# Kernel tuning notes

Measured on AMD Instinct MI355X. Metric: run time of the kernel, lower is better.

## Reference

```python
import jax, jax.numpy as jnp
import numpy as np

B, T, D_IN = 8, 1024, 320
L, H, DK, DV, DM, DI = 6, 8, 64, 64, 512, 2048


def _pe_table():
    pos = np.arange(T, dtype=np.float32)[:, None]
    div = np.exp(np.arange(0, DM, 2, dtype=np.float32) * (-np.log(10000.0) / DM))
    pe = np.zeros((T, DM), np.float32)
    pe[:, 0::2] = np.sin(pos * div)
    pe[:, 1::2] = np.cos(pos * div)
    return jnp.asarray(pe)


def setup_inputs() -> dict:
    key = jax.random.key(0)
    ks = jax.random.split(key, 16)
    rn = lambda k, shape, std: (jax.random.normal(k, shape, jnp.float32) * std)
    inp = {}
    inp["padded_input"] = jax.random.normal(ks[0], (B, T, D_IN), jnp.float32)
    inp["input_lengths"] = jax.random.randint(ks[1], (B,), T // 2, T + 1)
    # input projection + input layernorm (weights stored as [in, out])
    inp["w_in"] = rn(ks[2], (D_IN, DM), 0.02)
    inp["b_in"] = jnp.zeros((DM,), jnp.float32)
    inp["ln_in_g"] = jnp.ones((DM,), jnp.float32)
    inp["ln_in_b"] = jnp.zeros((DM,), jnp.float32)
    inp["pe"] = _pe_table()
    # stacked per-layer params, leading dim L
    inp["wq"] = rn(ks[3], (L, DM, H * DK), np.sqrt(2.0 / (DM + DK)))
    inp["bq"] = jnp.zeros((L, H * DK), jnp.float32)
    inp["wk"] = rn(ks[4], (L, DM, H * DK), np.sqrt(2.0 / (DM + DK)))
    inp["bk"] = jnp.zeros((L, H * DK), jnp.float32)
    inp["wv"] = rn(ks[5], (L, DM, H * DV), np.sqrt(2.0 / (DM + DV)))
    inp["bv"] = jnp.zeros((L, H * DV), jnp.float32)
    inp["wfc"] = rn(ks[6], (L, H * DV, DM), np.sqrt(2.0 / (H * DV + DM)))
    inp["bfc"] = jnp.zeros((L, DM), jnp.float32)
    inp["ln1_g"] = jnp.ones((L, DM), jnp.float32)
    inp["ln1_b"] = jnp.zeros((L, DM), jnp.float32)
    inp["w1"] = rn(ks[7], (L, DM, DI), np.sqrt(2.0 / (DM + DI)))
    inp["b1"] = jnp.zeros((L, DI), jnp.float32)
    inp["w2"] = rn(ks[8], (L, DI, DM), np.sqrt(2.0 / (DM + DI)))
    inp["b2"] = jnp.zeros((L, DM), jnp.float32)
    inp["ln2_g"] = jnp.ones((L, DM), jnp.float32)
    inp["ln2_b"] = jnp.zeros((L, DM), jnp.float32)
    return inp


def _layer_norm(x, g, b):
    mu = jnp.mean(x, axis=-1, keepdims=True)
    var = jnp.var(x, axis=-1, keepdims=True)
    return (x - mu) * jax.lax.rsqrt(var + 1e-5) * g + b


def _encoder(padded_input, input_lengths, w_in, b_in, ln_in_g, ln_in_b, pe,
             wq, bq, wk, bk, wv, bv, wfc, bfc, ln1_g, ln1_b,
             w1, b1, w2, b2, ln2_g, ln2_b):
    pos = jnp.arange(T)
    key_pad = pos[None, :] >= input_lengths[:, None]          # [B,T] True at pad
    non_pad = (~key_pad).astype(padded_input.dtype)[:, :, None]  # [B,T,1]
    scale = 1.0 / jnp.sqrt(jnp.float32(DK))

    x = _layer_norm(padded_input @ w_in + b_in, ln_in_g, ln_in_b) + pe[None]

    def body(x, p):
        Wq, Bq, Wk, Bk, Wv, Bv, Wfc, Bfc, G1, Bn1, W1, Bf1, W2, Bf2, G2, Bn2 = p
        res = x
        q = (x @ Wq + Bq).reshape(B, T, H, DK)
        k = (x @ Wk + Bk).reshape(B, T, H, DK)
        v = (x @ Wv + Bv).reshape(B, T, H, DV)
        attn = jnp.einsum('bqhd,bkhd->bhqk', q, k) * scale
        attn = jnp.where(key_pad[:, None, None, :], -jnp.inf, attn)
        attn = jax.nn.softmax(attn, axis=-1)
        o = jnp.einsum('bhqk,bkhd->bqhd', attn, v).reshape(B, T, H * DV)
        x = _layer_norm(o @ Wfc + Bfc + res, G1, Bn1) * non_pad
        res = x
        h = jax.nn.relu(x @ W1 + Bf1)
        x = _layer_norm(h @ W2 + Bf2 + res, G2, Bn2) * non_pad
        return x, None

    x, _ = jax.lax.scan(body, x, (wq, bq, wk, bk, wv, bv, wfc, bfc,
                                  ln1_g, ln1_b, w1, b1, w2, b2, ln2_g, ln2_b))
    return x


def reference(padded_input, input_lengths, w_in, b_in, ln_in_g, ln_in_b, pe,
              wq, bq, wk, bk, wv, bv, wfc, bfc, ln1_g, ln1_b,
              w1, b1, w2, b2, ln2_g, ln2_b):
    # dropout is identity in eval mode
    return _encoder(padded_input, input_lengths, w_in, b_in, ln_in_g, ln_in_b, pe,
                    wq, bq, wk, bk, wv, bv, wfc, bfc, ln1_g, ln1_b,
                    w1, b1, w2, b2, ln2_g, ln2_b)
```

## Files before the change

### kernel.cpp

```cpp
#include <hip/hip_runtime.h>
#include <hip/hip_bf16.h>


typedef unsigned short bh16;
typedef __bf16 bf16x8 __attribute__((ext_vector_type(8)));
typedef float f32x4 __attribute__((ext_vector_type(4)));
typedef unsigned int u32x4 __attribute__((ext_vector_type(4)));
typedef unsigned int u32x2 __attribute__((ext_vector_type(2)));

#define DEVI static __device__ __forceinline__

DEVI bh16 f2bf(float f) {
  union { float f; unsigned u; } x; x.f = f;
  unsigned r = x.u + 0x7fffu + ((x.u >> 16) & 1u);
  return (bh16)(r >> 16);
}
DEVI float bf2f(bh16 u) {
  union { unsigned u; float f; } x; x.u = ((unsigned)u) << 16; return x.f;
}
DEVI bf16x8 ld16(const bh16* p) {
  return __builtin_bit_cast(bf16x8, *(const u32x4*)p);
}
DEVI bf16x8 ld16b(const char* p) {
  return __builtin_bit_cast(bf16x8, *(const u32x4*)p);
}
DEVI f32x4 mfma16(bf16x8 a, bf16x8 b, f32x4 c) {
  return __builtin_amdgcn_mfma_f32_16x16x32_bf16(a, b, c, 0, 0, 0);
}
DEVI void async16(const void* g, void* l) {
  __builtin_amdgcn_global_load_lds(
      (const __attribute__((address_space(1))) void*)g,
      (__attribute__((address_space(3))) void*)l, 16, 0, 0);
}

__global__ __launch_bounds__(256) void tcvt(
    const float* __restrict__ in, bh16* __restrict__ out,
    int K, int N, long long inLS, long long outLS, int rowOff) {
  int l = blockIdx.z;
  in += (size_t)l * inLS;
  out += (size_t)l * outLS + (size_t)rowOff * K;
  __shared__ float t[32][33];
  int n0 = blockIdx.x * 32, k0 = blockIdx.y * 32;
  int tx = threadIdx.x & 31, ty = threadIdx.x >> 5;
#pragma unroll
  for (int i = 0; i < 4; i++)
    t[ty + 8 * i][tx] = in[(size_t)(k0 + ty + 8 * i) * N + n0 + tx];
  __syncthreads();
#pragma unroll
  for (int i = 0; i < 4; i++)
    out[(size_t)(n0 + ty + 8 * i) * K + k0 + tx] = f2bf(t[tx][ty + 8 * i]);
}

__global__ __launch_bounds__(256) void bcat(
    const float* __restrict__ bq, const float* __restrict__ bk,
    const float* __restrict__ bv, float* __restrict__ out) {
  int l = blockIdx.x;
  for (int j = threadIdx.x; j < 1536; j += 256) {
    float v = (j < 512) ? bq[l * 512 + j]
            : (j < 1024) ? bk[l * 512 + j - 512] : bv[l * 512 + j - 1024];
    out[l * 1536 + j] = v;
  }
}

__global__ __launch_bounds__(256) void cvt_in(
    const float* __restrict__ in, bh16* __restrict__ out, int n4) {
  int i = blockIdx.x * 256 + threadIdx.x;
  if (i < n4) {
    float4 v = ((const float4*)in)[i];
    u32x2 pk;
    pk[0] = (unsigned)f2bf(v.x) | ((unsigned)f2bf(v.y) << 16);
    pk[1] = (unsigned)f2bf(v.z) | ((unsigned)f2bf(v.w) << 16);
    *(u32x2*)(out + (size_t)i * 4) = pk;
  }
}

template <int RELU, int OUTF32, int QKV>
__global__ __launch_bounds__(256) void gemm_bt(
    const bh16* __restrict__ A, const bh16* __restrict__ Bt,
    const float* __restrict__ bias, void* __restrict__ Cout,
    bh16* __restrict__ vtOut, int M, int N, int K) {
  constexpr int BM = 128, BN = 64, BK = 64;
  __shared__ __align__(16) bh16 As[3][BM * BK];
  __shared__ __align__(16) bh16 Bs[3][BN * BK];
  const int tid = threadIdx.x;
  const int wave = tid >> 6, lane = tid & 63;
  const int lq = lane & 15, grp = lane >> 4;
  const int p = blockIdx.x;
  const int xcd = p & 7, idx = p >> 3;
  const int m0 = (((xcd << 3) | (idx & 7))) * BM;
  const int n0 = (idx >> 3) * BN;
  constexpr int FM = BM / 32, FN = BN / 32;
  const int wr = wave >> 1, wc = wave & 1;
  f32x4 acc[FM][FN] = {};

  const int nk = K / BK;
  auto stage = [&](int buf, int kt) {
#pragma unroll
    for (int i = 0; i < BM / 32; ++i) {
      int off = i * 4096 + wave * 1024 + lane * 16;
      int row = off >> 7, col = off & 127;
      int sw = (row & 7) << 4;
      const char* g =
          (const char*)A + ((size_t)(m0 + row) * K + kt * BK) * 2 + (col ^ sw);
      async16(g, (char*)As[buf] + off);
    }
#pragma unroll
    for (int i = 0; i < BN / 32; ++i) {
      int off = i * 4096 + wave * 1024 + lane * 16;
      int row = off >> 7, col = off & 127;
      int sw = (row & 7) << 4;
      const char* g =
          (const char*)Bt + ((size_t)(n0 + row) * K + kt * BK) * 2 + (col ^ sw);
      async16(g, (char*)Bs[buf] + off);
    }
  };

  stage(0, 0);
  stage(1, 1);
  int cur = 0, nxt = 2;
  for (int kt = 0; kt < nk; ++kt) {
    asm volatile("s_waitcnt vmcnt(6)" ::: "memory");
    __builtin_amdgcn_s_barrier();
    __builtin_amdgcn_sched_barrier(0);
    if (kt + 2 < nk) stage(nxt, kt + 2);
#pragma unroll
    for (int kk = 0; kk < 2; ++kk) {
      bf16x8 af[FM], bfr[FN];
#pragma unroll
      for (int i = 0; i < FM; ++i) {
        int row = wr * (BM / 2) + i * 16 + lq;
        int sw = (row & 7) << 4;
        af[i] = ld16b((char*)As[cur] + row * 128 + ((kk * 64 + grp * 16) ^ sw));
      }
#pragma unroll
      for (int j = 0; j < FN; ++j) {
        int row = wc * (BN / 2) + j * 16 + lq;
        int sw = (row & 7) << 4;
        bfr[j] = ld16b((char*)Bs[cur] + row * 128 + ((kk * 64 + grp * 16) ^ sw));
      }
      __builtin_amdgcn_s_setprio(1);
#pragma unroll
      for (int i = 0; i < FM; ++i)
#pragma unroll
        for (int j = 0; j < FN; ++j)
          acc[i][j] = mfma16(af[i], bfr[j], acc[i][j]);
      __builtin_amdgcn_s_setprio(0);
    }
    cur = (cur == 2) ? 0 : cur + 1;
    nxt = (nxt == 2) ? 0 : nxt + 1;
  }
  if (QKV && n0 >= 1024) {
#pragma unroll
    for (int i = 0; i < FM; ++i) {
#pragma unroll
      for (int j = 0; j < FN; ++j) {
        int col = n0 + wc * (BN / 2) + j * 16 + lq;
        float bv = bias[col];
        int vc = col - 1024;
        int t0 = m0 + wr * (BM / 2) + i * 16 + grp * 4;
        int bb = t0 >> 10, tl = t0 & 1023;
        u32x2 pk;
        pk[0] = (unsigned)f2bf(acc[i][j][0] + bv) |
                ((unsigned)f2bf(acc[i][j][1] + bv) << 16);
        pk[1] = (unsigned)f2bf(acc[i][j][2] + bv) |
                ((unsigned)f2bf(acc[i][j][3] + bv) << 16);
        *(u32x2*)&vtOut[((size_t)(bb * 512 + vc)) * 1024 + tl] = pk;
      }
    }
    return;
  }
#pragma unroll
  for (int i = 0; i < FM; ++i) {
#pragma unroll
    for (int j = 0; j < FN; ++j) {
      int col = n0 + wc * (BN / 2) + j * 16 + lq;
      float bv = bias[col];
#pragma unroll
      for (int r = 0; r < 4; ++r) {
        int row = m0 + wr * (BM / 2) + i * 16 + grp * 4 + r;
        float v = acc[i][j][r] + bv;
        if (RELU) v = fmaxf(v, 0.f);
        if (OUTF32) ((float*)Cout)[(size_t)row * N + col] = v;
        else ((bh16*)Cout)[(size_t)row * N + col] = f2bf(v);
      }
    }
  }
}

__global__ __launch_bounds__(256) void ln_pe_k(
    const float* __restrict__ in, const float* __restrict__ g,
    const float* __restrict__ bta, const float* __restrict__ pe,
    bh16* __restrict__ xb) {
  int wave = threadIdx.x >> 6, lane = threadIdx.x & 63;
  int row = blockIdx.x * 4 + wave;
  int t = row & 1023;
  const float* xr = in + (size_t)row * 512 + lane * 8;
  float4 a0 = ((const float4*)xr)[0], a1 = ((const float4*)xr)[1];
  float v[8] = {a0.x, a0.y, a0.z, a0.w, a1.x, a1.y, a1.z, a1.w};
  float s = 0.f, ss = 0.f;
#pragma unroll
  for (int j = 0; j < 8; j++) { s += v[j]; ss += v[j] * v[j]; }
#pragma unroll
  for (int m = 1; m < 64; m <<= 1) { s += __shfl_xor(s, m); ss += __shfl_xor(ss, m); }
  float mu = s * (1.f / 512.f);
  float rstd = rsqrtf(ss * (1.f / 512.f) - mu * mu + 1e-5f);
  int c0 = lane * 8;
  float o[8];
  u32x4 pk;
#pragma unroll
  for (int j = 0; j < 8; j++) {
    int c = c0 + j;
    o[j] = (v[j] - mu) * rstd * g[c] + bta[c] + pe[(size_t)t * 512 + c];
  }
#pragma unroll
  for (int j = 0; j < 4; j++)
    pk[j] = (unsigned)f2bf(o[2 * j]) | ((unsigned)f2bf(o[2 * j + 1]) << 16);
  *(u32x4*)(xb + (size_t)row * 512 + c0) = pk;
}

__global__ __launch_bounds__(256) void ln_res_k(
    const bh16* __restrict__ gout, const bh16* res,
    const float* __restrict__ g, const float* __restrict__ bta,
    const int* __restrict__ lens, bh16* xb, float* fout) {
  int wave = threadIdx.x >> 6, lane = threadIdx.x & 63;
  int row = blockIdx.x * 4 + wave;
  int b = row >> 10, t = row & 1023;
  float nonpad = (t < lens[b]) ? 1.f : 0.f;
  int c0 = lane * 8;
  u32x4 graw = *(const u32x4*)(gout + (size_t)row * 512 + c0);
  u32x4 rraw = *(const u32x4*)(res + (size_t)row * 512 + c0);
  float v[8];
#pragma unroll
  for (int j = 0; j < 4; j++) {
    v[2 * j] = bf2f((bh16)(graw[j] & 0xffffu)) + bf2f((bh16)(rraw[j] & 0xffffu));
    v[2 * j + 1] = bf2f((bh16)(graw[j] >> 16)) + bf2f((bh16)(rraw[j] >> 16));
  }
  float s = 0.f, ss = 0.f;
#pragma unroll
  for (int j = 0; j < 8; j++) { s += v[j]; ss += v[j] * v[j]; }
#pragma unroll
  for (int m = 1; m < 64; m <<= 1) { s += __shfl_xor(s, m); ss += __shfl_xor(ss, m); }
  float mu = s * (1.f / 512.f);
  float rstd = rsqrtf(ss * (1.f / 512.f) - mu * mu + 1e-5f);
  float o[8];
  u32x4 pk;
#pragma unroll
  for (int j = 0; j < 8; j++) {
    int c = c0 + j;
    o[j] = ((v[j] - mu) * rstd * g[c] + bta[c]) * nonpad;
  }
#pragma unroll
  for (int j = 0; j < 4; j++)
    pk[j] = (unsigned)f2bf(o[2 * j]) | ((unsigned)f2bf(o[2 * j + 1]) << 16);
  *(u32x4*)(xb + (size_t)row * 512 + c0) = pk;
  if (fout) {
    float4* xo = (float4*)(fout + (size_t)row * 512 + c0);
    xo[0] = make_float4(o[0], o[1], o[2], o[3]);
    xo[1] = make_float4(o[4], o[5], o[6], o[7]);
  }
}

__global__ __launch_bounds__(512) void attn_k(
    const bh16* __restrict__ qkv, const bh16* __restrict__ vt,
    const int* __restrict__ lens, bh16* __restrict__ o) {
  constexpr int LDP = 72;
  __shared__ __align__(16) char Ks[2][8192];
  __shared__ __align__(16) char Vs[2][8192];
  __shared__ __align__(16) bh16 P[8][16 * LDP];
  int p = blockIdx.x;
  int xcd = p & 7, s = p >> 3;
  int bh = ((s & 7) << 3) | xcd;
  int qt = s >> 3;
  int b = bh >> 3, h = bh & 7;
  int len = lens[b];
  if (qt * 128 >= len) return;
  int tid = threadIdx.x;
  int wave = tid >> 6, lane = tid & 63;
  int lq = lane & 15, grp = lane >> 4;

  size_t qrow = (size_t)(b * 1024 + qt * 128 + wave * 16 + lq);
  const bh16* Qp = qkv + qrow * 1536 + h * 64;
  bf16x8 qf0 = ld16(Qp + grp * 8);
  bf16x8 qf1 = ld16(Qp + 32 + grp * 8);
  const char* Kbase = (const char*)(qkv + (size_t)(b * 1024) * 1536 + 512 + h * 64);
  const char* Vbase = (const char*)(vt + (size_t)(bh * 64) * 1024);
  bh16* Pw = P[wave];

  f32x4 oacc[4] = {};
  float m = -1e30f, lsum = 0.f;
  int nkb = (len + 63) >> 6;

  auto stage = [&](int buf, int kb) {
    int off = tid * 16;
    int row = off >> 7, cb = off & 127;
    int sw = (row & 7) << 4;
    async16(Kbase + (size_t)(kb * 64 + row) * 3072 + (cb ^ sw), Ks[buf] + off);
    async16(Vbase + (size_t)row * 2048 + kb * 128 + (cb ^ sw), Vs[buf] + off);
  };

  stage(0, 0);
  for (int kb = 0; kb < nkb; ++kb) {
    int cur = kb & 1;
    __syncthreads();
    if (kb + 1 < nkb) stage(cur ^ 1, kb + 1);
    int k64 = kb * 64;
    f32x4 st[4];
    __builtin_amdgcn_s_setprio(1);
#pragma unroll
    for (int sv = 0; sv < 4; ++sv) {
      int row = sv * 16 + lq, sw = (row & 7) << 4;
      const char* kp = Ks[cur] + row * 128;
      f32x4 z = {};
      z = mfma16(ld16b(kp + ((grp * 16) ^ sw)), qf0, z);
      z = mfma16(ld16b(kp + ((64 + grp * 16) ^ sw)), qf1, z);
      st[sv] = z;
    }
    __builtin_amdgcn_s_setprio(0);
    float tmax = -1e30f;
    if (k64 + 64 > len) {
#pragma unroll
      for (int sv = 0; sv < 4; ++sv)
#pragma unroll
        for (int r = 0; r < 4; ++r) {
          int key = k64 + sv * 16 + grp * 4 + r;
          float v = st[sv][r] * 0.125f;
          v = (key < len) ? v : -1e30f;
          st[sv][r] = v;
          tmax = fmaxf(tmax, v);
        }
    } else {
#pragma unroll
      for (int sv = 0; sv < 4; ++sv)
#pragma unroll
        for (int r = 0; r < 4; ++r) {
          float v = st[sv][r] * 0.125f;
          st[sv][r] = v;
          tmax = fmaxf(tmax, v);
        }
    }
    tmax = fmaxf(tmax, __shfl_xor(tmax, 16));
    tmax = fmaxf(tmax, __shfl_xor(tmax, 32));
    float newm = fmaxf(m, tmax);
    if (!__all(newm - m <= 8.f)) {
      float sc = __expf(m - newm);
      m = newm;
      lsum *= sc;
#pragma unroll
      for (int r = 0; r < 4; ++r) {
        float scr = __shfl(sc, grp * 4 + r);
#pragma unroll
        for (int dt = 0; dt < 4; ++dt) oacc[dt][r] *= scr;
      }
    }
    float rs = 0.f;
#pragma unroll
    for (int sv = 0; sv < 4; ++sv) {
      float p0 = __expf(st[sv][0] - m), p1 = __expf(st[sv][1] - m);
      float p2 = __expf(st[sv][2] - m), p3 = __expf(st[sv][3] - m);
      rs += (p0 + p1) + (p2 + p3);
      u32x2 pk;
      pk[0] = (unsigned)f2bf(p0) | ((unsigned)f2bf(p1) << 16);
      pk[1] = (unsigned)f2bf(p2) | ((unsigned)f2bf(p3) << 16);
      *(u32x2*)&Pw[lq * LDP + sv * 16 + grp * 4] = pk;
    }
    rs += __shfl_xor(rs, 16);
    rs += __shfl_xor(rs, 32);
    lsum += rs;
#pragma unroll
    for (int kk = 0; kk < 2; ++kk) {
      bf16x8 pa = ld16(Pw + lq * LDP + kk * 32 + grp * 8);
      __builtin_amdgcn_s_setprio(1);
#pragma unroll
      for (int dt = 0; dt < 4; ++dt) {
        int row = dt * 16 + lq, sw = (row & 7) << 4;
        bf16x8 vfr = ld16b(Vs[cur] + row * 128 + ((kk * 64 + grp * 16) ^ sw));
        oacc[dt] = mfma16(pa, vfr, oacc[dt]);
      }
      __builtin_amdgcn_s_setprio(0);
    }
  }
#pragma unroll
  for (int r = 0; r < 4; ++r) {
    float li = __shfl(lsum, grp * 4 + r);
    float inv = 1.f / li;
    int row = qt * 128 + wave * 16 + grp * 4 + r;
    bh16* orow = o + (size_t)(b * 1024 + row) * 512 + h * 64;
#pragma unroll
    for (int dt = 0; dt < 4; ++dt) orow[dt * 16 + lq] = f2bf(oacc[dt][r] * inv);
  }
}

extern "C" void kernel_launch(void* const* d_in, const int* in_sizes, int n_in,
                              void* d_out, int out_size, void* d_ws, size_t ws_size,
                              hipStream_t stream) {
  const float* padded = (const float*)d_in[0];
  const int* lens = (const int*)d_in[1];
  const float* w_in = (const float*)d_in[2];
  const float* b_in = (const float*)d_in[3];
  const float* ln_in_g = (const float*)d_in[4];
  const float* ln_in_b = (const float*)d_in[5];
  const float* pe = (const float*)d_in[6];
  const float* wq = (const float*)d_in[7];
  const float* bq = (const float*)d_in[8];
  const float* wk = (const float*)d_in[9];
  const float* bk = (const float*)d_in[10];
  const float* wv = (const float*)d_in[11];
  const float* bv = (const float*)d_in[12];
  const float* wfc = (const float*)d_in[13];
  const float* bfc = (const float*)d_in[14];
  const float* ln1_g = (const float*)d_in[15];
  const float* ln1_b = (const float*)d_in[16];
  const float* w1 = (const float*)d_in[17];
  const float* b1 = (const float*)d_in[18];
  const float* w2 = (const float*)d_in[19];
  const float* b2 = (const float*)d_in[20];
  const float* ln2_g = (const float*)d_in[21];
  const float* ln2_b = (const float*)d_in[22];

  char* ws = (char*)d_ws;
  size_t off = 0;
  auto alloc = [&](size_t bytes) -> char* {
    char* p = ws + off;
    off += (bytes + 255) & ~(size_t)255;
    return p;
  };
  bh16* WinT  = (bh16*)alloc((size_t)512 * 320 * 2);
  bh16* WqkvT = (bh16*)alloc((size_t)6 * 1536 * 512 * 2);
  bh16* WfcT  = (bh16*)alloc((size_t)6 * 512 * 512 * 2);
  bh16* W1T   = (bh16*)alloc((size_t)6 * 2048 * 512 * 2);
  bh16* W2T   = (bh16*)alloc((size_t)6 * 512 * 2048 * 2);
  float* bqkv = (float*)alloc((size_t)6 * 1536 * 4);
  bh16* xb    = (bh16*)alloc((size_t)8192 * 512 * 2);
  bh16* qkvb  = (bh16*)alloc((size_t)8192 * 1536 * 2);
  bh16* vt    = (bh16*)alloc((size_t)64 * 64 * 1024 * 2);
  bh16* ob    = (bh16*)alloc((size_t)8192 * 512 * 2);
  float* tmp32 = (float*)alloc((size_t)8192 * 512 * 4);
  bh16* tmp16 = (bh16*)alloc((size_t)8192 * 512 * 2);
  bh16* hbuf  = (bh16*)alloc((size_t)8192 * 2048 * 2);
  bh16* padb  = hbuf;
  if (off > ws_size) return;

  tcvt<<<dim3(16, 10, 1), 256, 0, stream>>>(w_in, WinT, 320, 512, 0, 0, 0);
  tcvt<<<dim3(16, 16, 6), 256, 0, stream>>>(wq, WqkvT, 512, 512, 512 * 512, 1536 * 512, 0);
  tcvt<<<dim3(16, 16, 6), 256, 0, stream>>>(wk, WqkvT, 512, 512, 512 * 512, 1536 * 512, 512);
  tcvt<<<dim3(16, 16, 6), 256, 0, stream>>>(wv, WqkvT, 512, 512, 512 * 512, 1536 * 512, 1024);
  tcvt<<<dim3(16, 16, 6), 256, 0, stream>>>(wfc, WfcT, 512, 512, 512 * 512, 512 * 512, 0);
  tcvt<<<dim3(64, 16, 6), 256, 0, stream>>>(w1, W1T, 512, 2048, (long long)512 * 2048, (long long)2048 * 512, 0);
  tcvt<<<dim3(16, 64, 6), 256, 0, stream>>>(w2, W2T, 2048, 512, (long long)2048 * 512, (long long)512 * 2048, 0);
  bcat<<<6, 256, 0, stream>>>(bq, bk, bv, bqkv);
  cvt_in<<<2560, 256, 0, stream>>>(padded, padb, 655360);

  gemm_bt<0, 1, 0><<<512, 256, 0, stream>>>(
      padb, WinT, b_in, tmp32, nullptr, 8192, 512, 320);
  ln_pe_k<<<2048, 256, 0, stream>>>(tmp32, ln_in_g, ln_in_b, pe, xb);

  for (int l = 0; l < 6; ++l) {
    gemm_bt<0, 0, 1><<<1536, 256, 0, stream>>>(
        xb, WqkvT + (size_t)l * 1536 * 512, bqkv + l * 1536, qkvb, vt,
        8192, 1536, 512);
    attn_k<<<512, 512, 0, stream>>>(qkvb, vt, lens, ob);
    gemm_bt<0, 0, 0><<<512, 256, 0, stream>>>(
        ob, WfcT + (size_t)l * 512 * 512, bfc + l * 512, tmp16, nullptr,
        8192, 512, 512);
    ln_res_k<<<2048, 256, 0, stream>>>(tmp16, xb, ln1_g + l * 512, ln1_b + l * 512,
                                       lens, xb, nullptr);
    gemm_bt<1, 0, 0><<<2048, 256, 0, stream>>>(
        xb, W1T + (size_t)l * 2048 * 512, b1 + l * 2048, hbuf, nullptr,
        8192, 2048, 512);
    gemm_bt<0, 0, 0><<<512, 256, 0, stream>>>(
        hbuf, W2T + (size_t)l * 512 * 2048, b2 + l * 512, tmp16, nullptr,
        8192, 512, 2048);
    ln_res_k<<<2048, 256, 0, stream>>>(tmp16, xb, ln2_g + l * 512, ln2_b + l * 512,
                                       lens, xb, (l == 5) ? (float*)d_out : nullptr);
  }
}
```

Before: 869.8 us.

## Skip padded row tiles in GEMMs, enlarge tiles, simplify to double-buffered pipeline

The GEMM kernel now reads the sequence lengths and makes a block exit early when its row tile starts beyond that batch's valid length. Padded rows are masked or zeroed later, so this avoids wasted matrix work on them. Tile sizes become template parameters, with 128x128 tiles for the QKV and FFN1 GEMMs to cut launch count and improve operand reuse. The block-to-row mapping is reordered, and the 3-stage async pipeline with explicit vmcnt waits is replaced by a simpler 2-stage double buffer synchronized with __syncthreads. This risks less latency hiding, and it leaves padded-row buffers such as V^T unwritten, so stale data there must never produce NaN.

```diff
diff --git a/kernel.cpp b/kernel.cpp
--- a/kernel.cpp
+++ b/kernel.cpp
@@ -74,21 +74,23 @@
   }
 }
 
-template <int RELU, int OUTF32, int QKV>
+template <int BM, int BN, int RELU, int OUTF32, int QKV>
 __global__ __launch_bounds__(256) void gemm_bt(
     const bh16* __restrict__ A, const bh16* __restrict__ Bt,
     const float* __restrict__ bias, void* __restrict__ Cout,
-    bh16* __restrict__ vtOut, int M, int N, int K) {
-  constexpr int BM = 128, BN = 64, BK = 64;
-  __shared__ __align__(16) bh16 As[3][BM * BK];
-  __shared__ __align__(16) bh16 Bs[3][BN * BK];
+    bh16* __restrict__ vtOut, const int* __restrict__ lens,
+    int M, int N, int K) {
+  constexpr int BK = 64;
+  __shared__ __align__(16) bh16 As[2][BM * BK];
+  __shared__ __align__(16) bh16 Bs[2][BN * BK];
   const int tid = threadIdx.x;
   const int wave = tid >> 6, lane = tid & 63;
   const int lq = lane & 15, grp = lane >> 4;
   const int p = blockIdx.x;
   const int xcd = p & 7, idx = p >> 3;
-  const int m0 = (((xcd << 3) | (idx & 7))) * BM;
+  const int m0 = ((((idx & 7) << 3) | xcd)) * BM;
   const int n0 = (idx >> 3) * BN;
+  if ((m0 & 1023) >= lens[m0 >> 10]) return;
   constexpr int FM = BM / 32, FN = BN / 32;
   const int wr = wave >> 1, wc = wave & 1;
   f32x4 acc[FM][FN] = {};
@@ -116,13 +118,10 @@
   };
 
   stage(0, 0);
-  stage(1, 1);
-  int cur = 0, nxt = 2;
   for (int kt = 0; kt < nk; ++kt) {
-    asm volatile("s_waitcnt vmcnt(6)" ::: "memory");
-    __builtin_amdgcn_s_barrier();
-    __builtin_amdgcn_sched_barrier(0);
-    if (kt + 2 < nk) stage(nxt, kt + 2);
+    int cur = kt & 1;
+    __syncthreads();
+    if (kt + 1 < nk) stage(cur ^ 1, kt + 1);
 #pragma unroll
     for (int kk = 0; kk < 2; ++kk) {
       bf16x8 af[FM], bfr[FN];
@@ -146,8 +145,6 @@
           acc[i][j] = mfma16(af[i], bfr[j], acc[i][j]);
       __builtin_amdgcn_s_setprio(0);
     }
-    cur = (cur == 2) ? 0 : cur + 1;
-    nxt = (nxt == 2) ? 0 : nxt + 1;
   }
   if (QKV && n0 >= 1024) {
 #pragma unroll
@@ -450,25 +447,25 @@
   bcat<<<6, 256, 0, stream>>>(bq, bk, bv, bqkv);
   cvt_in<<<2560, 256, 0, stream>>>(padded, padb, 655360);
 
-  gemm_bt<0, 1, 0><<<512, 256, 0, stream>>>(
-      padb, WinT, b_in, tmp32, nullptr, 8192, 512, 320);
+  gemm_bt<128, 64, 0, 1, 0><<<512, 256, 0, stream>>>(
+      padb, WinT, b_in, tmp32, nullptr, lens, 8192, 512, 320);
   ln_pe_k<<<2048, 256, 0, stream>>>(tmp32, ln_in_g, ln_in_b, pe, xb);
 
   for (int l = 0; l < 6; ++l) {
-    gemm_bt<0, 0, 1><<<1536, 256, 0, stream>>>(
-        xb, WqkvT + (size_t)l * 1536 * 512, bqkv + l * 1536, qkvb, vt,
+    gemm_bt<128, 128, 0, 0, 1><<<768, 256, 0, stream>>>(
+        xb, WqkvT + (size_t)l * 1536 * 512, bqkv + l * 1536, qkvb, vt, lens,
         8192, 1536, 512);
     attn_k<<<512, 512, 0, stream>>>(qkvb, vt, lens, ob);
-    gemm_bt<0, 0, 0><<<512, 256, 0, stream>>>(
-        ob, WfcT + (size_t)l * 512 * 512, bfc + l * 512, tmp16, nullptr,
+    gemm_bt<128, 64, 0, 0, 0><<<512, 256, 0, stream>>>(
+        ob, WfcT + (size_t)l * 512 * 512, bfc + l * 512, tmp16, nullptr, lens,
         8192, 512, 512);
     ln_res_k<<<2048, 256, 0, stream>>>(tmp16, xb, ln1_g + l * 512, ln1_b + l * 512,
                                        lens, xb, nullptr);
-    gemm_bt<1, 0, 0><<<2048, 256, 0, stream>>>(
-        xb, W1T + (size_t)l * 2048 * 512, b1 + l * 2048, hbuf, nullptr,
+    gemm_bt<128, 128, 1, 0, 0><<<1024, 256, 0, stream>>>(
+        xb, W1T + (size_t)l * 2048 * 512, b1 + l * 2048, hbuf, nullptr, lens,
         8192, 2048, 512);
-    gemm_bt<0, 0, 0><<<512, 256, 0, stream>>>(
-        hbuf, W2T + (size_t)l * 512 * 2048, b2 + l * 512, tmp16, nullptr,
+    gemm_bt<128, 64, 0, 0, 0><<<512, 256, 0, stream>>>(
+        hbuf, W2T + (size_t)l * 512 * 2048, b2 + l * 512, tmp16, nullptr, lens,
         8192, 512, 2048);
     ln_res_k<<<2048, 256, 0, stream>>>(tmp16, xb, ln2_g + l * 512, ln2_b + l * 512,
                                        lens, xb, (l == 5) ? (float*)d_out : nullptr);
```

After: 823.0 us. -5.4%, faster.
